# Kernel optimization log

Measured on AMD Instinct MI355X. Metric: run time of the kernel, lower is better.

## Reference

```python
import jax, jax.numpy as jnp
import numpy as np

TEACHER_DIM = 512
STUDENT_DIM = 64
CHUNK_SIZE = TEACHER_DIM // STUDENT_DIM  # 8
NUM_CHUNKS = TEACHER_DIM // CHUNK_SIZE   # 64
B, H, W = 8, 96, 96


def setup_inputs() -> dict:
    key = jax.random.key(0)
    ks = jax.random.split(key, 7)
    x = jax.random.normal(ks[0], (B, TEACHER_DIM, H, W), dtype=jnp.float32)
    # stacked 1x1-conv weights: [num_chunks, out_ch, in_ch] and biases [num_chunks, out_ch]
    Wq = jax.random.normal(ks[1], (NUM_CHUNKS, CHUNK_SIZE, CHUNK_SIZE), dtype=jnp.float32)
    bq = jax.random.normal(ks[2], (NUM_CHUNKS, CHUNK_SIZE), dtype=jnp.float32)
    Wk = jax.random.normal(ks[3], (NUM_CHUNKS, CHUNK_SIZE, CHUNK_SIZE), dtype=jnp.float32)
    bk = jax.random.normal(ks[4], (NUM_CHUNKS, CHUNK_SIZE), dtype=jnp.float32)
    Wv = jax.random.normal(ks[5], (NUM_CHUNKS, CHUNK_SIZE, CHUNK_SIZE), dtype=jnp.float32)
    bv = jax.random.normal(ks[6], (NUM_CHUNKS, CHUNK_SIZE), dtype=jnp.float32)
    return {"x": x, "Wq": Wq, "bq": bq, "Wk": Wk, "bk": bk, "Wv": Wv, "bv": bv}


def reference(x, Wq, bq, Wk, bk, Wv, bv):
    b, c, h, w = x.shape
    hw = h * w
    # split channels into chunks -> [B, num_chunks, chunk_size, H*W]
    xc = x.reshape(b, NUM_CHUNKS, CHUNK_SIZE, hw)
    # 1x1 conv == per-chunk channel matmul; o=out_ch, c=in_ch, p=pixels
    q = jnp.einsum('bncp,noc->bnop', xc, Wq) + bq[None, :, :, None]
    k = jnp.einsum('bncp,noc->bnop', xc, Wk) + bk[None, :, :, None]
    v = jnp.einsum('bncp,noc->bnop', xc, Wv) + bv[None, :, :, None]
    # channel-attention: scores [B, num_chunks, chunk_size, chunk_size]
    scale = 1.0 / jnp.sqrt(jnp.asarray(hw, dtype=x.dtype))
    attn = jax.nn.softmax(jnp.einsum('bnqp,bnkp->bnqk', q, k) * scale, axis=-1)
    attended = jnp.einsum('bnqk,bnkp->bnqp', attn, v)  # [B,N,C,HW]
    # pooled = sum over chunk_size of elementwise product -> [B, num_chunks, H, W]
    pooled = jnp.sum(xc * attended, axis=2).reshape(b, NUM_CHUNKS, h, w)
    return pooled
```

## Files before the change

### kernel.cpp

```cpp
#include <hip/hip_runtime.h>

#define CHUNK 8
#define NCHUNK 64
#define TDIM 512
#define HW 9216
#define NT 256
#define F4_PER_CH (HW/4)
#define ITERS (F4_PER_CH/NT)

typedef float floatx4 __attribute__((ext_vector_type(4)));

__host__ __device__ constexpr int TRI(int c, int j) {
    return (c*(15-c))/2 + j;
}
__host__ __device__ constexpr int PairIdx(int c, int j) {
    return 7*c - (c*(c-1))/2 + (j - c - 1);
}

__device__ __forceinline__ unsigned bf16_rne(float f) {
    unsigned u = __float_as_uint(f);
    return (u + 0x7fffu + ((u >> 16) & 1u)) >> 16;
}
__device__ __forceinline__ float bf16_to_f(unsigned h16) {
    return __uint_as_float(h16 << 16);
}

__global__ __launch_bounds__(NT, 1)
void lcsap_kernel(const float* __restrict__ x,
                  const float* __restrict__ Wq, const float* __restrict__ bq,
                  const float* __restrict__ Wk, const float* __restrict__ bk,
                  const float* __restrict__ Wv, const float* __restrict__ bv,
                  float* __restrict__ out)
{
    const int bid = blockIdx.x;
    const int b   = bid >> 6;
    const int n   = bid & 63;
    const int tid = threadIdx.x;
    const int lane = tid & 63;
    const int wid  = tid >> 6;

    const float* xb = x + ((size_t)(b*TDIM + n*CHUNK)) * HW;
    float* ob = out + ((size_t)(b*NCHUNK + n)) * HW;

    __shared__ uint2 xs[8][F4_PER_CH];
    __shared__ float red[4][44];
    __shared__ float Gf[64];
    __shared__ float sf[8];
    __shared__ float Mld[64];
    __shared__ float tld[8];

    float g[36], sr[8];
    #pragma unroll
    for (int i = 0; i < 36; ++i) g[i] = 0.f;
    #pragma unroll
    for (int c = 0; c < 8; ++c) sr[c] = 0.f;

    floatx4 cur[8], nxt[8];
    #pragma unroll
    for (int c = 0; c < 8; ++c)
        cur[c] = reinterpret_cast<const floatx4*>(xb + (size_t)c*HW)[tid];

    #pragma unroll
    for (int it = 0; it < ITERS; ++it) {
        const int f = tid + it*NT;
        if (it + 1 < ITERS) {
            const int fn = f + NT;
            #pragma unroll
            for (int c = 0; c < 8; ++c)
                nxt[c] = reinterpret_cast<const floatx4*>(xb + (size_t)c*HW)[fn];
        }
        #pragma unroll
        for (int c = 0; c < 8; ++c) {
            uint2 p;
            p.x = bf16_rne(cur[c][0]) | (bf16_rne(cur[c][1]) << 16);
            p.y = bf16_rne(cur[c][2]) | (bf16_rne(cur[c][3]) << 16);
            xs[c][f] = p;
        }
        #pragma unroll
        for (int u = 0; u < 4; ++u) {
            float xv[8];
            #pragma unroll
            for (int c = 0; c < 8; ++c) xv[c] = cur[c][u];
            #pragma unroll
            for (int c = 0; c < 8; ++c) sr[c] += xv[c];
            #pragma unroll
            for (int c = 0; c < 8; ++c) {
                #pragma unroll
                for (int j = c; j < 8; ++j)
                    g[TRI(c,j)] += xv[c]*xv[j];
            }
        }
        #pragma unroll
        for (int c = 0; c < 8; ++c) cur[c] = nxt[c];
    }

    #pragma unroll
    for (int i = 0; i < 36; ++i) {
        g[i] += __shfl_xor(g[i], 1);  g[i] += __shfl_xor(g[i], 2);
        g[i] += __shfl_xor(g[i], 4);  g[i] += __shfl_xor(g[i], 8);
        g[i] += __shfl_xor(g[i], 16); g[i] += __shfl_xor(g[i], 32);
    }
    #pragma unroll
    for (int c = 0; c < 8; ++c) {
        sr[c] += __shfl_xor(sr[c], 1);  sr[c] += __shfl_xor(sr[c], 2);
        sr[c] += __shfl_xor(sr[c], 4);  sr[c] += __shfl_xor(sr[c], 8);
        sr[c] += __shfl_xor(sr[c], 16); sr[c] += __shfl_xor(sr[c], 32);
    }
    if (lane == 0) {
        #pragma unroll
        for (int i = 0; i < 36; ++i) red[wid][i] = g[i];
        #pragma unroll
        for (int c = 0; c < 8; ++c) red[wid][36+c] = sr[c];
    }
    __syncthreads();
    if (tid < 44) {
        float v = red[0][tid] + red[1][tid] + red[2][tid] + red[3][tid];
        if (tid < 36) {
            int c = 0, base = 0;
            for (; c < 8; ++c) { int w = 8 - c; if (tid < base + w) break; base += w; }
            int j = c + (tid - base);
            Gf[c*8+j] = v;
            Gf[j*8+c] = v;
        } else {
            sf[tid-36] = v;
        }
    }
    __syncthreads();

    if (tid < 64) {
        const int qi = tid >> 3;
        const int ki = tid & 7;
        float wq[8], wk[8];
        #pragma unroll
        for (int c = 0; c < 8; ++c) {
            wq[c] = Wq[n*64 + qi*8 + c];
            wk[c] = Wk[n*64 + ki*8 + c];
        }
        float sc = 0.f, qs = 0.f, ks_ = 0.f;
        #pragma unroll
        for (int c = 0; c < 8; ++c) {
            float tmp = 0.f;
            #pragma unroll
            for (int d = 0; d < 8; ++d) tmp += Gf[c*8+d]*wk[d];
            sc += wq[c]*tmp;
            qs += wq[c]*sf[c];
            ks_ += wk[c]*sf[c];
        }
        const float bqv = bq[n*8+qi];
        const float bkv = bk[n*8+ki];
        sc += qs*bkv + bqv*ks_ + (float)HW * bqv * bkv;
        sc *= (1.0f/96.0f);

        float m = sc;
        m = fmaxf(m, __shfl_xor(m, 1, 8));
        m = fmaxf(m, __shfl_xor(m, 2, 8));
        m = fmaxf(m, __shfl_xor(m, 4, 8));
        float e = expf(sc - m);
        float se = e;
        se += __shfl_xor(se, 1, 8);
        se += __shfl_xor(se, 2, 8);
        se += __shfl_xor(se, 4, 8);
        const float attn = e / se;

        float mv = 0.f;
        #pragma unroll
        for (int k = 0; k < 8; ++k) {
            float ak = __shfl(attn, k, 8);
            mv += ak * Wv[n*64 + k*8 + ki];
        }
        Mld[qi*8 + ki] = mv;

        float tv = attn * bv[n*8 + ki];
        tv += __shfl_xor(tv, 1, 8);
        tv += __shfl_xor(tv, 2, 8);
        tv += __shfl_xor(tv, 4, 8);
        if (ki == 0) tld[qi] = tv;
    }
    __syncthreads();

    float diag[8], tt[8], su[28];
    #pragma unroll
    for (int c = 0; c < 8; ++c) { diag[c] = Mld[c*9]; tt[c] = tld[c]; }
    #pragma unroll
    for (int c = 0; c < 8; ++c) {
        #pragma unroll
        for (int j = c+1; j < 8; ++j)
            su[PairIdx(c,j)] = Mld[c*8+j] + Mld[j*8+c];
    }

    #pragma unroll
    for (int it = 0; it < ITERS; ++it) {
        const int f = tid + it*NT;
        uint2 v[8];
        #pragma unroll
        for (int c = 0; c < 8; ++c) v[c] = xs[c][f];
        floatx4 o;
        #pragma unroll
        for (int u = 0; u < 4; ++u) {
            float xv[8];
            #pragma unroll
            for (int c = 0; c < 8; ++c) {
                unsigned w32 = (u < 2) ? v[c].x : v[c].y;
                unsigned h   = (u & 1) ? (w32 >> 16) : (w32 & 0xffffu);
                xv[c] = bf16_to_f(h);
            }
            float acc = 0.f;
            #pragma unroll
            for (int c = 0; c < 8; ++c) acc += tt[c]*xv[c];
            #pragma unroll
            for (int c = 0; c < 8; ++c) acc += diag[c]*xv[c]*xv[c];
            #pragma unroll
            for (int c = 0; c < 8; ++c) {
                #pragma unroll
                for (int j = c+1; j < 8; ++j)
                    acc += su[PairIdx(c,j)]*xv[c]*xv[j];
            }
            o[u] = acc;
        }
        reinterpret_cast<floatx4*>(ob)[f] = o;
    }
}

extern "C" void kernel_launch(void* const* d_in, const int* in_sizes, int n_in,
                              void* d_out, int out_size, void* d_ws, size_t ws_size,
                              hipStream_t stream) {
    const float* x  = (const float*)d_in[0];
    const float* Wq = (const float*)d_in[1];
    const float* bq = (const float*)d_in[2];
    const float* Wk = (const float*)d_in[3];
    const float* bk = (const float*)d_in[4];
    const float* Wv = (const float*)d_in[5];
    const float* bv = (const float*)d_in[6];
    float* out = (float*)d_out;

    lcsap_kernel<<<dim3(512), dim3(NT), 0, stream>>>(x, Wq, bq, Wk, bk, Wv, bv, out);
}
```

Before: 51.45 us.

## Keep bf16-packed input in registers instead of LDS to raise occupancy

The bf16-compressed copy of the 8-channel chunk now stays in registers (144 dwords per thread) rather than in a 72KB shared-memory buffer. Without that LDS footprint, launch bounds change to allow two blocks per CU, so the latency-bound streaming phase can overlap across blocks. The register double buffer is also rewritten as ping-pong qA/qB with no copy, and the bf16 unpack uses a mask instead of a shift. The cost is very high register pressure: 144 packed values plus 72 prefetch registers plus accumulators could cause spills or stop the second block from fitting.

```diff
diff --git a/kernel.cpp b/kernel.cpp
--- a/kernel.cpp
+++ b/kernel.cpp
@@ -5,8 +5,8 @@
 #define TDIM 512
 #define HW 9216
 #define NT 256
-#define F4_PER_CH (HW/4)
-#define ITERS (F4_PER_CH/NT)
+#define F4C 2304
+#define K9 9
 
 typedef float floatx4 __attribute__((ext_vector_type(4)));
 
@@ -21,11 +21,8 @@
     unsigned u = __float_as_uint(f);
     return (u + 0x7fffu + ((u >> 16) & 1u)) >> 16;
 }
-__device__ __forceinline__ float bf16_to_f(unsigned h16) {
-    return __uint_as_float(h16 << 16);
-}
-
-__global__ __launch_bounds__(NT, 1)
+
+__global__ __launch_bounds__(NT, 2)
 void lcsap_kernel(const float* __restrict__ x,
                   const float* __restrict__ Wq, const float* __restrict__ bq,
                   const float* __restrict__ Wk, const float* __restrict__ bk,
@@ -42,12 +39,11 @@
     const float* xb = x + ((size_t)(b*TDIM + n*CHUNK)) * HW;
     float* ob = out + ((size_t)(b*NCHUNK + n)) * HW;
 
-    __shared__ uint2 xs[8][F4_PER_CH];
     __shared__ float red[4][44];
+    __shared__ float Mld[64];
+    __shared__ float tld[8];
     __shared__ float Gf[64];
     __shared__ float sf[8];
-    __shared__ float Mld[64];
-    __shared__ float tld[8];
 
     float g[36], sr[8];
     #pragma unroll
@@ -55,34 +51,40 @@
     #pragma unroll
     for (int c = 0; c < 8; ++c) sr[c] = 0.f;
 
-    floatx4 cur[8], nxt[8];
+    unsigned d[8][K9][2];
+
+    floatx4 qA[8], qB[8];
     #pragma unroll
     for (int c = 0; c < 8; ++c)
-        cur[c] = reinterpret_cast<const floatx4*>(xb + (size_t)c*HW)[tid];
-
-    #pragma unroll
-    for (int it = 0; it < ITERS; ++it) {
-        const int f = tid + it*NT;
-        if (it + 1 < ITERS) {
-            const int fn = f + NT;
-            #pragma unroll
-            for (int c = 0; c < 8; ++c)
-                nxt[c] = reinterpret_cast<const floatx4*>(xb + (size_t)c*HW)[fn];
-        }
-        #pragma unroll
-        for (int c = 0; c < 8; ++c) {
-            uint2 p;
-            p.x = bf16_rne(cur[c][0]) | (bf16_rne(cur[c][1]) << 16);
-            p.y = bf16_rne(cur[c][2]) | (bf16_rne(cur[c][3]) << 16);
-            xs[c][f] = p;
+        qA[c] = reinterpret_cast<const floatx4*>(xb + (size_t)c*HW)[tid];
+
+    #pragma unroll
+    for (int k = 0; k < K9; ++k) {
+        if (k + 1 < K9) {
+            const int fn = tid + (k+1)*NT;
+            if (k & 1) {
+                #pragma unroll
+                for (int c = 0; c < 8; ++c)
+                    qA[c] = reinterpret_cast<const floatx4*>(xb + (size_t)c*HW)[fn];
+            } else {
+                #pragma unroll
+                for (int c = 0; c < 8; ++c)
+                    qB[c] = reinterpret_cast<const floatx4*>(xb + (size_t)c*HW)[fn];
+            }
+        }
+        #pragma unroll
+        for (int c = 0; c < 8; ++c) {
+            floatx4 v = (k & 1) ? qB[c] : qA[c];
+            #pragma unroll
+            for (int u = 0; u < 4; ++u) sr[c] += v[u];
+            d[c][k][0] = bf16_rne(v[0]) | (bf16_rne(v[1]) << 16);
+            d[c][k][1] = bf16_rne(v[2]) | (bf16_rne(v[3]) << 16);
         }
         #pragma unroll
         for (int u = 0; u < 4; ++u) {
             float xv[8];
             #pragma unroll
-            for (int c = 0; c < 8; ++c) xv[c] = cur[c][u];
-            #pragma unroll
-            for (int c = 0; c < 8; ++c) sr[c] += xv[c];
+            for (int c = 0; c < 8; ++c) xv[c] = (k & 1) ? qB[c][u] : qA[c][u];
             #pragma unroll
             for (int c = 0; c < 8; ++c) {
                 #pragma unroll
@@ -90,8 +92,6 @@
                     g[TRI(c,j)] += xv[c]*xv[j];
             }
         }
-        #pragma unroll
-        for (int c = 0; c < 8; ++c) cur[c] = nxt[c];
     }
 
     #pragma unroll
@@ -141,7 +141,7 @@
         for (int c = 0; c < 8; ++c) {
             float tmp = 0.f;
             #pragma unroll
-            for (int d = 0; d < 8; ++d) tmp += Gf[c*8+d]*wk[d];
+            for (int dd = 0; dd < 8; ++dd) tmp += Gf[c*8+dd]*wk[dd];
             sc += wq[c]*tmp;
             qs += wq[c]*sf[c];
             ks_ += wk[c]*sf[c];
@@ -189,35 +189,33 @@
     }
 
     #pragma unroll
-    for (int it = 0; it < ITERS; ++it) {
-        const int f = tid + it*NT;
-        uint2 v[8];
-        #pragma unroll
-        for (int c = 0; c < 8; ++c) v[c] = xs[c][f];
+    for (int k = 0; k < K9; ++k) {
+        float xv[8][4];
+        #pragma unroll
+        for (int c = 0; c < 8; ++c) {
+            const unsigned w0 = d[c][k][0], w1 = d[c][k][1];
+            xv[c][0] = __uint_as_float(w0 << 16);
+            xv[c][1] = __uint_as_float(w0 & 0xffff0000u);
+            xv[c][2] = __uint_as_float(w1 << 16);
+            xv[c][3] = __uint_as_float(w1 & 0xffff0000u);
+        }
         floatx4 o;
         #pragma unroll
         for (int u = 0; u < 4; ++u) {
-            float xv[8];
+            float acc = 0.f;
+            #pragma unroll
+            for (int c = 0; c < 8; ++c) acc += tt[c]*xv[c][u];
+            #pragma unroll
+            for (int c = 0; c < 8; ++c) acc += diag[c]*xv[c][u]*xv[c][u];
             #pragma unroll
             for (int c = 0; c < 8; ++c) {
-                unsigned w32 = (u < 2) ? v[c].x : v[c].y;
-                unsigned h   = (u & 1) ? (w32 >> 16) : (w32 & 0xffffu);
-                xv[c] = bf16_to_f(h);
-            }
-            float acc = 0.f;
-            #pragma unroll
-            for (int c = 0; c < 8; ++c) acc += tt[c]*xv[c];
-            #pragma unroll
-            for (int c = 0; c < 8; ++c) acc += diag[c]*xv[c]*xv[c];
-            #pragma unroll
-            for (int c = 0; c < 8; ++c) {
                 #pragma unroll
                 for (int j = c+1; j < 8; ++j)
-                    acc += su[PairIdx(c,j)]*xv[c]*xv[j];
+                    acc += su[PairIdx(c,j)]*xv[c][u]*xv[j][u];
             }
             o[u] = acc;
         }
-        reinterpret_cast<floatx4*>(ob)[f] = o;
+        reinterpret_cast<floatx4*>(ob)[tid + k*NT] = o;
     }
 }
 
```

After: 80.32 us. +56.1%, slower.
